# Optimization experiments

Hardware: AMD Instinct MI355X
Metric: run time of the kernel (lower is better)

The kernel has to match this reference:

```python
import jax, jax.numpy as jnp
import numpy as np

B, C, H, W = 4, 32, 64, 64
K = 3
HEADS = 8
SF = 4
D = C * K * K          # 288, unfold token dim
E = D // 2             # 144, reduced dim
DH = E // HEADS        # 18, head dim
SCALE = DH ** -0.5
N = H * W              # 4096 tokens


def unfold(x):
    # x: (B,C,H,W) -> (B, C*K*K, H*W), torch.nn.Unfold ordering (c, kh, kw)
    xp = jnp.pad(x, ((0, 0), (0, 0), (1, 1), (1, 1)))
    patches = jnp.stack([xp[:, :, i:i + H, j:j + W] for i in range(K) for j in range(K)], axis=2)
    return patches.reshape(x.shape[0], C * K * K, H * W)


def fold(cols):
    # inverse of unfold: scatter-add overlapping patches back, crop padding
    b = cols.shape[0]
    y = cols.reshape(b, C, K, K, H, W)
    out = jnp.zeros((b, C, H + 2, W + 2), cols.dtype)
    for i in range(K):
        for j in range(K):
            out = out.at[:, :, i:i + H, j:j + W].add(y[:, :, i, j])
    return out[:, :, 1:-1, 1:-1]


def layernorm_cols(cols, g, b):
    # LayerNorm over D applied on (B,N,D) view, returned as (B,D,N)
    xt = cols.transpose(0, 2, 1)
    mu = xt.mean(-1, keepdims=True)
    var = xt.var(-1, keepdims=True)
    y = (xt - mu) / jnp.sqrt(var + 1e-5) * g + b
    return y.transpose(0, 2, 1)


def emha(x, wr, br, wqkv, we, be):
    # x: (B, D, N)
    b, _, n_tok = x.shape
    xr = jnp.einsum('bdn,ed->ben', x, wr) + br[None, :, None]   # Conv1d k=1 reduction
    t = xr.transpose(0, 2, 1)                                   # (B,N,E)
    qkv = t @ wqkv.T                                            # Linear, no bias
    q, k, v = jnp.split(qkv, 3, axis=-1)
    n = n_tok // SF

    def rs(a):
        return a.reshape(b, n_tok, HEADS, DH).transpose(0, 2, 1, 3).reshape(b, HEADS, SF, n, DH)

    q, k, v = rs(q), rs(k), rs(v)
    attn = jax.nn.softmax(jnp.einsum('bhsnd,bhsmd->bhsnm', q, k) * SCALE, axis=-1)
    o = jnp.einsum('bhsnm,bhsmd->bhsnd', attn, v)
    o = o.reshape(b, HEADS, n_tok, DH).transpose(0, 2, 1, 3).reshape(b, n_tok, E).transpose(0, 2, 1)
    return jnp.einsum('ben,fe->bfn', o, we) + be[None, :, None]  # Conv1d k=1 expansion


def conv3x3(x, w, b):
    y = jax.lax.conv_general_dilated(x, w, (1, 1), ((1, 1), (1, 1)),
                                     dimension_numbers=('NCHW', 'OIHW', 'NCHW'))
    return y + b[None, :, None, None]


def setup_inputs() -> dict:
    key = jax.random.key(0)
    ks = jax.random.split(key, 20)
    s = 0.02
    inp = {
        'x': jax.random.normal(ks[0], (B, C, H, W), jnp.float32),
        'ln_g': jnp.ones((D,), jnp.float32),
        'ln_b': jnp.zeros((D,), jnp.float32),
        'conv_w': jax.random.normal(ks[1], (C, C, 3, 3), jnp.float32) * s,
        'conv_b': jnp.zeros((C,), jnp.float32),
    }
    for i in range(3):
        k0, k1, k2 = jax.random.split(ks[2 + i], 3)
        inp[f'wr{i+1}'] = jax.random.normal(k0, (E, D), jnp.float32) * s
        inp[f'br{i+1}'] = jnp.zeros((E,), jnp.float32)
        inp[f'wqkv{i+1}'] = jax.random.normal(k1, (3 * E, E), jnp.float32) * s
        inp[f'we{i+1}'] = jax.random.normal(k2, (D, E), jnp.float32) * s
        inp[f'be{i+1}'] = jnp.zeros((D,), jnp.float32)
    return inp


def reference(x, ln_g, ln_b, conv_w, conv_b,
              wr1, br1, wqkv1, we1, be1,
              wr2, br2, wqkv2, we2, be2,
              wr3, br3, wqkv3, we3, be3):
    t = x
    for (wr, br, wqkv, we, be) in ((wr1, br1, wqkv1, we1, be1),
                                   (wr2, br2, wqkv2, we2, be2),
                                   (wr3, br3, wqkv3, we3, be3)):
        cols = unfold(t)
        cols_n = layernorm_cols(cols, ln_g, ln_b)
        cols = emha(cols_n, wr, br, wqkv, we, be) + cols
        t = fold(cols)
    return x + jax.nn.elu(conv3x3(t, conv_w, conv_b))
```

## Files before the change

kernel.cpp:

```cpp
#include <hip/hip_runtime.h>
#include <math.h>

#define BN 4
#define CC 32
#define HH 64
#define WW 64
#define DD 288
#define EE 144
#define NTOK 4096
#define SCALE_F 0.2357022603955158f
#define QSCALE  0.3401074286f
#define QKST 384
#define MQKV 528

typedef __bf16 bf16x8 __attribute__((ext_vector_type(8)));
typedef float floatx4 __attribute__((ext_vector_type(4)));
typedef unsigned short u16x8 __attribute__((ext_vector_type(8)));

__device__ __forceinline__ unsigned short f2bf(float x) {
    unsigned int u = __float_as_uint(x);
    u += 0x7fffu + ((u >> 16) & 1u);
    return (unsigned short)(u >> 16);
}
__device__ __forceinline__ float bf2f(unsigned short s) {
    return __uint_as_float(((unsigned int)s) << 16);
}
__device__ __forceinline__ unsigned int pack_bf_trunc(float a, float b) {
    return __builtin_amdgcn_perm(__float_as_uint(b), __float_as_uint(a), 0x07060302u);
}
__device__ __forceinline__ void plswap32(unsigned int& a, unsigned int& b) {
    asm("v_permlane32_swap_b32 %0, %1" : "+v"(a), "+v"(b));
}
__device__ __forceinline__ void plswap16(unsigned int& a, unsigned int& b) {
    asm("v_permlane16_swap_b32 %0, %1" : "+v"(a), "+v"(b));
}

__global__ __launch_bounds__(256) void setup_k(
    const float* __restrict__ wr0, const float* __restrict__ br0,
    const float* __restrict__ wr1, const float* __restrict__ br1,
    const float* __restrict__ wr2, const float* __restrict__ br2,
    const float* __restrict__ g,  const float* __restrict__ lb,
    const float* __restrict__ wqkv0, const float* __restrict__ wqkv1, const float* __restrict__ wqkv2,
    const float* __restrict__ we0,   const float* __restrict__ we1,   const float* __restrict__ we2,
    unsigned short* __restrict__ wg_bf, float* __restrict__ wgsum, float* __restrict__ wbeta,
    unsigned short* __restrict__ wqkv_bf, unsigned short* __restrict__ we_bf)
{
    int blk = blockIdx.x;
    int tid = threadIdx.x;
    if (blk < 3) {
        if (tid < 144) {
            int l = blk, e = tid;
            const float* wr = (l == 0) ? wr0 : ((l == 1) ? wr1 : wr2);
            const float* br = (l == 0) ? br0 : ((l == 1) ? br1 : br2);
            float sg = 0.f, sb = 0.f;
            for (int d = 0; d < DD; ++d) {
                float w = wr[e * DD + d];
                float wgv = w * g[d];
                wg_bf[((size_t)l * EE + e) * DD + d] = f2bf(wgv);
                sg += wgv;
                sb += w * lb[d];
            }
            wgsum[l * EE + e] = sg;
            wbeta[l * EE + e] = sb + br[e];
        }
        return;
    }
    int idx = (blk - 3) * 256 + tid;
    const int T1 = 3 * MQKV * 160;
    const int T2 = 3 * 288 * 160;
    if (idx < T1) {
        int l = idx / (MQKV * 160), r = idx % (MQKV * 160);
        int m = r / 160, k = r % 160;
        const float* w = (l == 0) ? wqkv0 : ((l == 1) ? wqkv1 : wqkv2);
        float v = 0.f;
        if (k < 144) {
            if (m < 192) {
                int h = m / 24, j = m % 24;
                if (j < 18) v = w[(h * 18 + j) * 144 + k] * QSCALE;
            } else if (m < 384) {
                int mm = m - 192, h = mm / 24, j = mm % 24;
                if (j < 18) v = w[(144 + h * 18 + j) * 144 + k];
            } else {
                v = w[(288 + (m - 384)) * 144 + k];
            }
        }
        wqkv_bf[idx] = f2bf(v);
    } else if (idx < T1 + T2) {
        int j = idx - T1;
        int l = j / (288 * 160), r = j % (288 * 160);
        int m = r / 160, k = r % 160;
        const float* w = (l == 0) ? we0 : ((l == 1) ? we1 : we2);
        we_bf[j] = (k < 144) ? f2bf(w[m * 144 + k]) : 0;
    }
}

__global__ __launch_bounds__(256) void unfold_k(const float* __restrict__ t,
    unsigned short* __restrict__ colsT,
    float* __restrict__ mu, float* __restrict__ rstd)
{
    __shared__ float red1[4][64], red2[4][64];
    int tid = threadIdx.x;
    int lane = tid & 63, cpart = tid >> 6;
    int b = blockIdx.x >> 6, nc = blockIdx.x & 63;
    int n = nc * 64 + lane;
    int h = n >> 6, w = n & 63;
    const float* tb = t + (size_t)b * CC * HH * WW;
    unsigned short loc[72];
    float s1 = 0.f, s2 = 0.f;
    #pragma unroll
    for (int c8 = 0; c8 < 8; ++c8) {
        int c = cpart * 8 + c8;
        const float* tc = tb + (size_t)c * 4096;
        #pragma unroll
        for (int i = 0; i < 3; ++i) {
            int hr = h + i - 1;
            bool rok = ((unsigned)hr < 64u);
            #pragma unroll
            for (int j = 0; j < 3; ++j) {
                int wc = w + j - 1;
                bool ok = rok && ((unsigned)wc < 64u);
                float v = ok ? tc[hr * 64 + wc] : 0.f;
                loc[c8 * 9 + i * 3 + j] = f2bf(v);
                s1 += v;
                s2 = fmaf(v, v, s2);
            }
        }
    }
    unsigned short* ct = colsT + ((size_t)b * NTOK + n) * 288 + cpart * 72;
    #pragma unroll
    for (int u = 0; u < 9; ++u)
        *(u16x8*)&ct[u * 8] = *(const u16x8*)&loc[u * 8];
    red1[cpart][lane] = s1;
    red2[cpart][lane] = s2;
    __syncthreads();
    if (tid < 64) {
        float a = red1[0][tid] + red1[1][tid] + red1[2][tid] + red1[3][tid];
        float q = red2[0][tid] + red2[1][tid] + red2[2][tid] + red2[3][tid];
        float m = a * (1.f / 288.f);
        float var = q * (1.f / 288.f) - m * m;
        int nn = nc * 64 + tid;
        mu[b * NTOK + nn] = m;
        rstd[b * NTOK + nn] = rsqrtf(var + 1e-5f);
    }
}

template<int K, int MODE, int NYB>
__global__ __launch_bounds__(256) void mgemm_k(
    const unsigned short* __restrict__ A, const unsigned short* __restrict__ Bt, int BST,
    unsigned short* __restrict__ Ct, unsigned short* __restrict__ Cv,
    const float* __restrict__ mu, const float* __restrict__ rstd,
    const float* __restrict__ wgsum, const float* __restrict__ wbeta,
    const float* __restrict__ bias)
{
    constexpr int NT = 64;
    __shared__ unsigned short Ts[64 * 56];
    int flat = blockIdx.x;
    int g  = (flat / (8 * NYB)) * 8 + (flat & 7);
    int jm = (flat % (8 * NYB)) >> 3;
    int n0 = (g & 63) * NT;
    int bI = g >> 6;
    int m0 = jm * 48;
    int tid = threadIdx.x;
    int wv = tid >> 6, lane = tid & 63;
    int l15 = lane & 15, l4 = lane >> 4;

    const unsigned short* Arow = A + (size_t)(m0 + l15) * K + l4 * 8;
    const unsigned short* Brow = Bt + ((size_t)bI * NTOK + n0 + wv * 16 + l15) * BST + l4 * 8;

    floatx4 acc[3];
    acc[0] = acc[1] = acc[2] = (floatx4){0.f, 0.f, 0.f, 0.f};

    #pragma unroll
    for (int ks = 0; ks < K / 32; ++ks) {
        bf16x8 bfr = *(const bf16x8*)(Brow + ks * 32);
        #pragma unroll
        for (int mi = 0; mi < 3; ++mi) {
            bf16x8 af = *(const bf16x8*)(Arow + (size_t)mi * 16 * K + ks * 32);
            acc[mi] = __builtin_amdgcn_mfma_f32_16x16x32_bf16(af, bfr, acc[mi], 0, 0, 0);
        }
    }

    int n_l = wv * 16 + l15;

    if (MODE == 2) {
        #pragma unroll
        for (int mi = 0; mi < 3; ++mi)
            #pragma unroll
            for (int r = 0; r < 4; ++r) {
                int m_l = mi * 16 + l4 * 4 + r;
                Ts[m_l * 72 + n_l] = f2bf(acc[mi][r] + bias[m0 + m_l]);
            }
        __syncthreads();
        for (int u = tid; u < 48 * 8; u += 256) {
            int row = u >> 3, seg = u & 7;
            unsigned short* dst = Ct + ((size_t)bI * DD + m0 + row) * NTOK + n0 + seg * 8;
            *(u16x8*)dst = *(const u16x8*)&Ts[row * 72 + seg * 8];
        }
    } else {
        bool vpath = (MODE == 0) && (m0 >= 384);
        float muv = 0.f, rsv = 0.f;
        if (MODE == 1) {
            int n_g = n0 + n_l;
            muv = mu[bI * NTOK + n_g];
            rsv = rstd[bI * NTOK + n_g];
        }
        #pragma unroll
        for (int mi = 0; mi < 3; ++mi)
            #pragma unroll
            for (int r = 0; r < 4; ++r) {
                int m_l = mi * 16 + l4 * 4 + r;
                float v = acc[mi][r];
                if (MODE == 1) v = rsv * (v - muv * wgsum[m0 + m_l]) + wbeta[m0 + m_l];
                if (!vpath) Ts[n_l * 56 + m_l] = f2bf(v);
                else        Ts[m_l * 72 + n_l] = f2bf(v);
            }
        __syncthreads();
        if (!vpath) {
            const int CTS = (MODE == 1) ? 160 : QKST;
            if (tid < 128) {
                int row = tid >> 1, half = tid & 1;
                unsigned short* dst = Ct + ((size_t)bI * NTOK + n0 + row) * CTS + m0 + half * 24;
                const unsigned short* src = &Ts[row * 56 + half * 24];
                #pragma unroll
                for (int u = 0; u < 3; ++u)
                    *(u16x8*)&dst[u * 8] = *(const u16x8*)&src[u * 8];
                if (MODE == 1 && m0 == 96) {
                    u16x8 z = (u16x8)0;
                    *(u16x8*)(Ct + ((size_t)bI * NTOK + n0 + row) * 160 + 144 + half * 8) = z;
                }
            }
        } else {
            for (int u = tid; u < 48 * 8; u += 256) {
                int row = u >> 3, seg = u & 7;
                unsigned short* dst = Cv + ((size_t)bI * EE + (m0 - 384) + row) * NTOK + n0 + seg * 8;
                *(u16x8*)dst = *(const u16x8*)&Ts[row * 72 + seg * 8];
            }
        }
    }
}

__global__ __launch_bounds__(256, 6) void attn_k2(const unsigned short* __restrict__ qkT,
                                                  const unsigned short* __restrict__ vF,
                                                  unsigned short* __restrict__ oT)
{
    __shared__ unsigned short Ks[128 * 40];
    __shared__ unsigned short Vs[32 * 136];

    int blk = blockIdx.x;
    int bhs = blk & 127;
    int qc  = blk >> 7;
    int b = bhs >> 5, h = (bhs >> 2) & 7, s = bhs & 3;
    int tid  = threadIdx.x;
    int wv   = tid >> 6;
    int lane = tid & 63;
    int l15 = lane & 15, l4 = lane >> 4;
    int q0 = qc * 64;
    int tokbase = s * 1024;

    const unsigned short* qkb = qkT + (size_t)b * NTOK * QKST;

    if (tid < 128) {
        u16x8 z = (u16x8)0;
        *(u16x8*)&Ks[tid * 40 + 24] = z;
    } else {
        for (int v = tid - 128; v < 14 * 16; v += 128) {
            int d = 18 + (v >> 4), seg = v & 15;
            unsigned short val = (d == 31) ? (unsigned short)0x3F80 : (unsigned short)0;
            u16x8 vv = (u16x8)val;
            *(u16x8*)&Vs[d * 136 + seg * 8] = vv;
        }
    }

    bf16x8 qf;
    {
        u16x8 raw = *(const u16x8*)(qkb + (size_t)(tokbase + q0 + wv * 16 + l15) * QKST
                                    + 24 * h + l4 * 8);
        if (l4 == 3) raw = (u16x8)0;
        qf = *(bf16x8*)&raw;
    }

    floatx4 oacc[2];
    oacc[0] = (floatx4){0.f, 0.f, 0.f, 0.f};
    oacc[1] = (floatx4){0.f, 0.f, 0.f, 0.f};

    u16x8 preg[3];
    int vb = tid - 128;
    bool v3 = (vb < 32);
    if (tid < 128) {
        const unsigned short* src = qkb + (size_t)(tokbase + tid) * QKST + 192 + 24 * h;
        preg[0] = *(const u16x8*)&src[0];
        preg[1] = *(const u16x8*)&src[8];
        preg[2] = *(const u16x8*)&src[16];
    } else {
        const unsigned short* vbb = vF + (size_t)b * EE * NTOK + tokbase;
        #pragma unroll
        for (int u = 0; u < 3; ++u) {
            int idx = vb + u * 128;
            if (u < 2 || v3) {
                int d = idx >> 4, seg = idx & 15;
                preg[u] = *(const u16x8*)(vbb + (size_t)(h * 18 + d) * NTOK + seg * 8);
            }
        }
    }

    for (int c0 = 0; c0 < 1024; c0 += 128) {
        __syncthreads();
        if (tid < 128) {
            unsigned short* dk = &Ks[tid * 40];
            *(u16x8*)&dk[0]  = preg[0];
            *(u16x8*)&dk[8]  = preg[1];
            *(u16x8*)&dk[16] = preg[2];
        } else {
            #pragma unroll
            for (int u = 0; u < 3; ++u) {
                int idx = vb + u * 128;
                if (u < 2 || v3) {
                    int d = idx >> 4, seg = idx & 15;
                    *(u16x8*)&Vs[d * 136 + seg * 8] = preg[u];
                }
            }
        }
        int cn = c0 + 128;
        if (cn < 1024) {
            if (tid < 128) {
                const unsigned short* src = qkb + (size_t)(tokbase + cn + tid) * QKST + 192 + 24 * h;
                preg[0] = *(const u16x8*)&src[0];
                preg[1] = *(const u16x8*)&src[8];
                preg[2] = *(const u16x8*)&src[16];
            } else {
                const unsigned short* vbb = vF + (size_t)b * EE * NTOK + tokbase + cn;
                #pragma unroll
                for (int u = 0; u < 3; ++u) {
                    int idx = vb + u * 128;
                    if (u < 2 || v3) {
                        int d = idx >> 4, seg = idx & 15;
                        preg[u] = *(const u16x8*)(vbb + (size_t)(h * 18 + d) * NTOK + seg * 8);
                    }
                }
            }
        }
        __syncthreads();

        #pragma unroll
        for (int sub = 0; sub < 2; ++sub) {
            bf16x8 kf[4];
            #pragma unroll
            for (int mi = 0; mi < 4; ++mi)
                kf[mi] = *(const bf16x8*)&Ks[(sub * 64 + mi * 16 + l15) * 40 + l4 * 8];

            floatx4 sacc[4];
            #pragma unroll
            for (int mi = 0; mi < 4; ++mi) {
                floatx4 z = (floatx4){0.f, 0.f, 0.f, 0.f};
                sacc[mi] = __builtin_amdgcn_mfma_f32_16x16x32_bf16(kf[mi], qf, z, 0, 0, 0);
            }

            unsigned int pk0[4], pk1[4];
            #pragma unroll
            for (int mi = 0; mi < 4; ++mi) {
                pk0[mi] = pack_bf_trunc(exp2f(sacc[mi][0]), exp2f(sacc[mi][1]));
                pk1[mi] = pack_bf_trunc(exp2f(sacc[mi][2]), exp2f(sacc[mi][3]));
            }

            #pragma unroll
            for (int c = 0; c < 2; ++c) {
                unsigned int B0 = pk0[2 * c], B2 = pk0[2 * c + 1];
                unsigned int B1 = pk1[2 * c], B3 = pk1[2 * c + 1];
                plswap32(B0, B2); plswap16(B0, B2);
                plswap32(B1, B3); plswap16(B1, B3);
                union { unsigned int u[4]; bf16x8 v; } bfr;
                bfr.u[0] = B0; bfr.u[1] = B1; bfr.u[2] = B2; bfr.u[3] = B3;
                #pragma unroll
                for (int nd = 0; nd < 2; ++nd) {
                    bf16x8 af = *(const bf16x8*)&Vs[(nd * 16 + l15) * 136 + sub * 64 + c * 32 + l4 * 8];
                    oacc[nd] = __builtin_amdgcn_mfma_f32_16x16x32_bf16(af, bfr.v, oacc[nd], 0, 0, 0);
                }
            }
        }
    }

    float lsum = __shfl(oacc[1][3], 48 + l15, 64);
    float inv  = 1.f / lsum;
    size_t rowi = (size_t)b * NTOK + tokbase + q0 + wv * 16 + l15;
    unsigned short* orow = oT + rowi * 160 + h * 18;
    unsigned int w0 = (unsigned)f2bf(oacc[0][0] * inv) | ((unsigned)f2bf(oacc[0][1] * inv) << 16);
    unsigned int w1 = (unsigned)f2bf(oacc[0][2] * inv) | ((unsigned)f2bf(oacc[0][3] * inv) << 16);
    *(unsigned int*)&orow[l4 * 4]     = w0;
    *(unsigned int*)&orow[l4 * 4 + 2] = w1;
    if (l4 == 0) {
        unsigned int w2 = (unsigned)f2bf(oacc[1][0] * inv) | ((unsigned)f2bf(oacc[1][1] * inv) << 16);
        *(unsigned int*)&orow[16] = w2;
    }
    if (h == 7 && l4 < 2) {
        u16x8 z = (u16x8)0;
        *(u16x8*)(oT + rowi * 160 + 144 + l4 * 8) = z;
    }
}

__global__ __launch_bounds__(256) void fold_k(const unsigned short* __restrict__ cols,
                                              const float* __restrict__ tprev,
                                              float* __restrict__ t)
{
    int idx = blockIdx.x * 256 + threadIdx.x;
    int w = idx & 63;
    int h = (idx >> 6) & 63;
    int c = (idx >> 12) & 31;
    int b = idx >> 17;
    const unsigned short* cb = cols + (size_t)b * DD * NTOK + (size_t)c * 9 * NTOK;
    float sum = 0.f;
    #pragma unroll
    for (int i = 0; i < 3; ++i) {
        int hs = h + 1 - i;
        if ((unsigned)hs < 64u) {
            #pragma unroll
            for (int j = 0; j < 3; ++j) {
                int ws_ = w + 1 - j;
                if ((unsigned)ws_ < 64u)
                    sum += bf2f(cb[(size_t)(i * 3 + j) * NTOK + hs * 64 + ws_]);
            }
        }
    }
    int ch = (h == 0 || h == 63) ? 2 : 3;
    int cw_ = (w == 0 || w == 63) ? 2 : 3;
    t[idx] = sum + (float)(ch * cw_) * tprev[idx];
}

__global__ __launch_bounds__(256) void conv_k(const float* __restrict__ t,
    const float* __restrict__ cw, const float* __restrict__ cbias,
    const float* __restrict__ x, float* __restrict__ out)
{
    __shared__ float wsh[CC * 9];
    int blk = blockIdx.x;
    int band = blk & 3, co = (blk >> 2) & 31, b = blk >> 7;
    int tid = threadIdx.x;
    for (int u = tid; u < CC * 9; u += 256) wsh[u] = cw[co * CC * 9 + u];
    __syncthreads();
    int h = band * 16 + (tid >> 4);
    int w0 = (tid & 15) << 2;
    const float* tb = t + (size_t)b * CC * 4096;
    float bias = cbias[co];
    float a0 = bias, a1 = bias, a2 = bias, a3 = bias;
    for (int ci = 0; ci < CC; ++ci) {
        const float* tc = tb + (size_t)ci * 4096;
        const float* wr = &wsh[ci * 9];
        #pragma unroll
        for (int i = 0; i < 3; ++i) {
            int hr = h + i - 1;
            if ((unsigned)hr < 64u) {
                const float* row = tc + hr * 64;
                float vl = (w0 > 0)  ? row[w0 - 1] : 0.f;
                float4 c4 = *(const float4*)&row[w0];
                float vr = (w0 < 60) ? row[w0 + 4] : 0.f;
                float wj0 = wr[i * 3], wj1 = wr[i * 3 + 1], wj2 = wr[i * 3 + 2];
                a0 = fmaf(wj0, vl,   a0); a0 = fmaf(wj1, c4.x, a0); a0 = fmaf(wj2, c4.y, a0);
                a1 = fmaf(wj0, c4.x, a1); a1 = fmaf(wj1, c4.y, a1); a1 = fmaf(wj2, c4.z, a1);
                a2 = fmaf(wj0, c4.y, a2); a2 = fmaf(wj1, c4.z, a2); a2 = fmaf(wj2, c4.w, a2);
                a3 = fmaf(wj0, c4.z, a3); a3 = fmaf(wj1, c4.w, a3); a3 = fmaf(wj2, vr,   a3);
            }
        }
    }
    size_t oidx = ((size_t)(b * CC + co) * 4096) + h * 64 + w0;
    float4 xin = *(const float4*)&x[oidx];
    float4 o;
    o.x = xin.x + ((a0 > 0.f) ? a0 : (__expf(a0) - 1.f));
    o.y = xin.y + ((a1 > 0.f) ? a1 : (__expf(a1) - 1.f));
    o.z = xin.z + ((a2 > 0.f) ? a2 : (__expf(a2) - 1.f));
    o.w = xin.w + ((a3 > 0.f) ? a3 : (__expf(a3) - 1.f));
    *(float4*)&out[oidx] = o;
}

extern "C" void kernel_launch(void* const* d_in, const int* in_sizes, int n_in,
                              void* d_out, int out_size, void* d_ws, size_t ws_size,
                              hipStream_t stream)
{
    const float* x    = (const float*)d_in[0];
    const float* ln_g = (const float*)d_in[1];
    const float* ln_b = (const float*)d_in[2];
    const float* cw   = (const float*)d_in[3];
    const float* cb   = (const float*)d_in[4];
    const float* wr[3]   = {(const float*)d_in[5],  (const float*)d_in[10], (const float*)d_in[15]};
    const float* br[3]   = {(const float*)d_in[6],  (const float*)d_in[11], (const float*)d_in[16]};
    const float* wqkv[3] = {(const float*)d_in[7],  (const float*)d_in[12], (const float*)d_in[17]};
    const float* we[3]   = {(const float*)d_in[8],  (const float*)d_in[13], (const float*)d_in[18]};
    const float* be[3]   = {(const float*)d_in[9],  (const float*)d_in[14], (const float*)d_in[19]};
    float* out = (float*)d_out;

    char* p = (char*)d_ws;
    unsigned short* cols_bf = (unsigned short*)p; p += (size_t)BN * DD * NTOK * 2;
    unsigned short* colsT = (unsigned short*)p; p += (size_t)BN * NTOK * 288 * 2;
    unsigned short* oT = colsT;
    unsigned short* xrT   = (unsigned short*)p; p += (size_t)BN * NTOK * 160 * 2;
    unsigned short* qkT   = (unsigned short*)p; p += (size_t)BN * NTOK * QKST * 2;
    unsigned short* vF    = (unsigned short*)p; p += (size_t)BN * EE * NTOK * 2;
    float* mu   = (float*)p;              p += (size_t)BN * NTOK * 4;
    float* rstd = (float*)p;              p += (size_t)BN * NTOK * 4;
    float* tA   = (float*)p;              p += (size_t)BN * CC * HH * WW * 4;
    float* tB   = (float*)p;              p += (size_t)BN * CC * HH * WW * 4;
    unsigned short* wg_bf   = (unsigned short*)p; p += (size_t)3 * EE * DD * 2;
    unsigned short* wqkv_bf = (unsigned short*)p; p += (size_t)3 * MQKV * 160 * 2;
    unsigned short* we_bf   = (unsigned short*)p; p += (size_t)3 * DD * 160 * 2;
    float* wgsum = (float*)p;             p += 3 * EE * 4;
    float* wbeta = (float*)p;             p += 3 * EE * 4;
    (void)in_sizes; (void)n_in; (void)out_size; (void)ws_size;

    setup_k<<<1533, 256, 0, stream>>>(wr[0], br[0], wr[1], br[1], wr[2], br[2], ln_g, ln_b,
                                      wqkv[0], wqkv[1], wqkv[2], we[0], we[1], we[2],
                                      wg_bf, wgsum, wbeta, wqkv_bf, we_bf);

    const float* tin = x;
    float* touts[3] = {tA, tB, tA};
    for (int l = 0; l < 3; ++l) {
        unfold_k<<<256, 256, 0, stream>>>(tin, colsT, mu, rstd);
        mgemm_k<288, 1, 3><<<768, 256, 0, stream>>>(
            wg_bf + (size_t)l * EE * DD, colsT, 288, xrT, nullptr,
            mu, rstd, wgsum + l * EE, wbeta + l * EE, nullptr);
        mgemm_k<160, 0, 11><<<2816, 256, 0, stream>>>(
            wqkv_bf + (size_t)l * MQKV * 160, xrT, 160, qkT, vF,
            nullptr, nullptr, nullptr, nullptr, nullptr);
        attn_k2<<<2048, 256, 0, stream>>>(qkT, vF, oT);
        mgemm_k<160, 2, 6><<<1536, 256, 0, stream>>>(
            we_bf + (size_t)l * DD * 160, oT, 160, cols_bf, nullptr,
            nullptr, nullptr, nullptr, nullptr, be[l]);
        fold_k<<<2048, 256, 0, stream>>>(cols_bf, tin, touts[l]);
        tin = touts[l];
    }
    conv_k<<<512, 256, 0, stream>>>(tA, cw, cb, x, out);
}
```

Before: 432.1 us.

## Store K in per-head padded layout and load K fragments directly from global

The QKV GEMM now writes K into a separate per-(batch,head) buffer with a 32-element padded row, and Q into its own narrower buffer. The attention kernel reads K MFMA fragments straight from global memory into registers instead of staging them through shared memory, so only V goes through LDS and the K LDS buffer disappears. It also swaps exp2f for the hardware exp2 intrinsic and lowers the launch-bounds occupancy hint from 6 to 4 to make room for the extra registers. The cost is more global-load traffic per wave, since each of the four waves in a block re-reads the same K, and possibly lower occupancy.

```diff
diff --git a/kernel.cpp b/kernel.cpp
--- a/kernel.cpp
+++ b/kernel.cpp
@@ -10,7 +10,8 @@
 #define NTOK 4096
 #define SCALE_F 0.2357022603955158f
 #define QSCALE  0.3401074286f
-#define QKST 384
+#define QST 192
+#define KST 32
 #define MQKV 528
 
 typedef __bf16 bf16x8 __attribute__((ext_vector_type(8)));
@@ -147,7 +148,7 @@
 template<int K, int MODE, int NYB>
 __global__ __launch_bounds__(256) void mgemm_k(
     const unsigned short* __restrict__ A, const unsigned short* __restrict__ Bt, int BST,
-    unsigned short* __restrict__ Ct, unsigned short* __restrict__ Cv,
+    unsigned short* __restrict__ Ct, unsigned short* __restrict__ Cv, unsigned short* __restrict__ Ck,
     const float* __restrict__ mu, const float* __restrict__ rstd,
     const float* __restrict__ wgsum, const float* __restrict__ wbeta,
     const float* __restrict__ bias)
@@ -216,17 +217,26 @@
             }
         __syncthreads();
         if (!vpath) {
-            const int CTS = (MODE == 1) ? 160 : QKST;
             if (tid < 128) {
                 int row = tid >> 1, half = tid & 1;
-                unsigned short* dst = Ct + ((size_t)bI * NTOK + n0 + row) * CTS + m0 + half * 24;
                 const unsigned short* src = &Ts[row * 56 + half * 24];
-                #pragma unroll
-                for (int u = 0; u < 3; ++u)
-                    *(u16x8*)&dst[u * 8] = *(const u16x8*)&src[u * 8];
-                if (MODE == 1 && m0 == 96) {
-                    u16x8 z = (u16x8)0;
-                    *(u16x8*)(Ct + ((size_t)bI * NTOK + n0 + row) * 160 + 144 + half * 8) = z;
+                if (MODE == 0 && m0 >= 192) {
+                    int head = (m0 - 192) / 24 + half;
+                    unsigned short* dst = Ck + ((size_t)(bI * 8 + head) * NTOK + n0 + row) * KST;
+                    #pragma unroll
+                    for (int u = 0; u < 3; ++u)
+                        *(u16x8*)&dst[u * 8] = *(const u16x8*)&src[u * 8];
+                    *(u16x8*)&dst[24] = (u16x8)0;
+                } else {
+                    const int CTS = (MODE == 1) ? 160 : QST;
+                    unsigned short* dst = Ct + ((size_t)bI * NTOK + n0 + row) * CTS + m0 + half * 24;
+                    #pragma unroll
+                    for (int u = 0; u < 3; ++u)
+                        *(u16x8*)&dst[u * 8] = *(const u16x8*)&src[u * 8];
+                    if (MODE == 1 && m0 == 96) {
+                        u16x8 z = (u16x8)0;
+                        *(u16x8*)(Ct + ((size_t)bI * NTOK + n0 + row) * 160 + 144 + half * 8) = z;
+                    }
                 }
             }
         } else {
@@ -239,11 +249,11 @@
     }
 }
 
-__global__ __launch_bounds__(256, 6) void attn_k2(const unsigned short* __restrict__ qkT,
+__global__ __launch_bounds__(256, 4) void attn_k2(const unsigned short* __restrict__ qT,
+                                                  const unsigned short* __restrict__ kP,
                                                   const unsigned short* __restrict__ vF,
                                                   unsigned short* __restrict__ oT)
 {
-    __shared__ unsigned short Ks[128 * 40];
     __shared__ unsigned short Vs[32 * 136];
 
     int blk = blockIdx.x;
@@ -257,23 +267,16 @@
     int q0 = qc * 64;
     int tokbase = s * 1024;
 
-    const unsigned short* qkb = qkT + (size_t)b * NTOK * QKST;
-
-    if (tid < 128) {
-        u16x8 z = (u16x8)0;
-        *(u16x8*)&Ks[tid * 40 + 24] = z;
-    } else {
-        for (int v = tid - 128; v < 14 * 16; v += 128) {
-            int d = 18 + (v >> 4), seg = v & 15;
-            unsigned short val = (d == 31) ? (unsigned short)0x3F80 : (unsigned short)0;
-            u16x8 vv = (u16x8)val;
-            *(u16x8*)&Vs[d * 136 + seg * 8] = vv;
-        }
+    for (int v = tid; v < 14 * 16; v += 256) {
+        int d = 18 + (v >> 4), seg = v & 15;
+        unsigned short val = (d == 31) ? (unsigned short)0x3F80 : (unsigned short)0;
+        u16x8 vv = (u16x8)val;
+        *(u16x8*)&Vs[d * 136 + seg * 8] = vv;
     }
 
     bf16x8 qf;
     {
-        u16x8 raw = *(const u16x8*)(qkb + (size_t)(tokbase + q0 + wv * 16 + l15) * QKST
+        u16x8 raw = *(const u16x8*)(qT + ((size_t)b * NTOK + tokbase + q0 + wv * 16 + l15) * QST
                                     + 24 * h + l4 * 8);
         if (l4 == 3) raw = (u16x8)0;
         qf = *(bf16x8*)&raw;
@@ -283,83 +286,52 @@
     oacc[0] = (floatx4){0.f, 0.f, 0.f, 0.f};
     oacc[1] = (floatx4){0.f, 0.f, 0.f, 0.f};
 
-    u16x8 preg[3];
-    int vb = tid - 128;
-    bool v3 = (vb < 32);
-    if (tid < 128) {
-        const unsigned short* src = qkb + (size_t)(tokbase + tid) * QKST + 192 + 24 * h;
-        preg[0] = *(const u16x8*)&src[0];
-        preg[1] = *(const u16x8*)&src[8];
-        preg[2] = *(const u16x8*)&src[16];
-    } else {
-        const unsigned short* vbb = vF + (size_t)b * EE * NTOK + tokbase;
-        #pragma unroll
-        for (int u = 0; u < 3; ++u) {
-            int idx = vb + u * 128;
-            if (u < 2 || v3) {
-                int d = idx >> 4, seg = idx & 15;
-                preg[u] = *(const u16x8*)(vbb + (size_t)(h * 18 + d) * NTOK + seg * 8);
-            }
-        }
-    }
+    const unsigned short* vbb = vF + (size_t)b * EE * NTOK + tokbase;
+    int d0 = tid >> 4, seg0 = tid & 15;
+    bool x2 = (tid < 32);
+    int d1 = 16 + (tid >> 4), seg1 = tid & 15;
+    u16x8 pv0, pv1;
+    pv0 = *(const u16x8*)(vbb + (size_t)(h * 18 + d0) * NTOK + seg0 * 8);
+    if (x2) pv1 = *(const u16x8*)(vbb + (size_t)(h * 18 + d1) * NTOK + seg1 * 8);
+
+    const unsigned short* kRow = kP + ((size_t)(b * 8 + h) * NTOK + tokbase + l15) * KST + l4 * 8;
 
     for (int c0 = 0; c0 < 1024; c0 += 128) {
+        bf16x8 kreg[8];
+        #pragma unroll
+        for (int sub = 0; sub < 2; ++sub)
+            #pragma unroll
+            for (int mi = 0; mi < 4; ++mi) {
+                u16x8 raw = *(const u16x8*)(kRow + (unsigned)(c0 + sub * 64 + mi * 16) * KST);
+                kreg[sub * 4 + mi] = *(bf16x8*)&raw;
+            }
+
         __syncthreads();
-        if (tid < 128) {
-            unsigned short* dk = &Ks[tid * 40];
-            *(u16x8*)&dk[0]  = preg[0];
-            *(u16x8*)&dk[8]  = preg[1];
-            *(u16x8*)&dk[16] = preg[2];
-        } else {
-            #pragma unroll
-            for (int u = 0; u < 3; ++u) {
-                int idx = vb + u * 128;
-                if (u < 2 || v3) {
-                    int d = idx >> 4, seg = idx & 15;
-                    *(u16x8*)&Vs[d * 136 + seg * 8] = preg[u];
-                }
-            }
-        }
+        *(u16x8*)&Vs[d0 * 136 + seg0 * 8] = pv0;
+        if (x2) *(u16x8*)&Vs[d1 * 136 + seg1 * 8] = pv1;
         int cn = c0 + 128;
         if (cn < 1024) {
-            if (tid < 128) {
-                const unsigned short* src = qkb + (size_t)(tokbase + cn + tid) * QKST + 192 + 24 * h;
-                preg[0] = *(const u16x8*)&src[0];
-                preg[1] = *(const u16x8*)&src[8];
-                preg[2] = *(const u16x8*)&src[16];
-            } else {
-                const unsigned short* vbb = vF + (size_t)b * EE * NTOK + tokbase + cn;
-                #pragma unroll
-                for (int u = 0; u < 3; ++u) {
-                    int idx = vb + u * 128;
-                    if (u < 2 || v3) {
-                        int d = idx >> 4, seg = idx & 15;
-                        preg[u] = *(const u16x8*)(vbb + (size_t)(h * 18 + d) * NTOK + seg * 8);
-                    }
-                }
-            }
+            pv0 = *(const u16x8*)(vbb + (size_t)(h * 18 + d0) * NTOK + cn + seg0 * 8);
+            if (x2) pv1 = *(const u16x8*)(vbb + (size_t)(h * 18 + d1) * NTOK + cn + seg1 * 8);
         }
         __syncthreads();
 
         #pragma unroll
         for (int sub = 0; sub < 2; ++sub) {
-            bf16x8 kf[4];
-            #pragma unroll
-            for (int mi = 0; mi < 4; ++mi)
-                kf[mi] = *(const bf16x8*)&Ks[(sub * 64 + mi * 16 + l15) * 40 + l4 * 8];
-
             floatx4 sacc[4];
             #pragma unroll
             for (int mi = 0; mi < 4; ++mi) {
                 floatx4 z = (floatx4){0.f, 0.f, 0.f, 0.f};
-                sacc[mi] = __builtin_amdgcn_mfma_f32_16x16x32_bf16(kf[mi], qf, z, 0, 0, 0);
+                sacc[mi] = __builtin_amdgcn_mfma_f32_16x16x32_bf16(kreg[sub * 4 + mi], qf, z, 0, 0, 0);
             }
 
             unsigned int pk0[4], pk1[4];
             #pragma unroll
             for (int mi = 0; mi < 4; ++mi) {
-                pk0[mi] = pack_bf_trunc(exp2f(sacc[mi][0]), exp2f(sacc[mi][1]));
-                pk1[mi] = pack_bf_trunc(exp2f(sacc[mi][2]), exp2f(sacc[mi][3]));
+                pk0[mi] = pack_bf_trunc(__builtin_amdgcn_exp2f(sacc[mi][0]),
+                                        __builtin_amdgcn_exp2f(sacc[mi][1]));
+                pk1[mi] = pack_bf_trunc(__builtin_amdgcn_exp2f(sacc[mi][2]),
+                                        __builtin_amdgcn_exp2f(sacc[mi][3]));
             }
 
             #pragma unroll
@@ -490,7 +462,8 @@
     unsigned short* colsT = (unsigned short*)p; p += (size_t)BN * NTOK * 288 * 2;
     unsigned short* oT = colsT;
     unsigned short* xrT   = (unsigned short*)p; p += (size_t)BN * NTOK * 160 * 2;
-    unsigned short* qkT   = (unsigned short*)p; p += (size_t)BN * NTOK * QKST * 2;
+    unsigned short* qT    = (unsigned short*)p; p += (size_t)BN * NTOK * QST * 2;
+    unsigned short* kP    = (unsigned short*)p; p += (size_t)BN * 8 * NTOK * KST * 2;
     unsigned short* vF    = (unsigned short*)p; p += (size_t)BN * EE * NTOK * 2;
     float* mu   = (float*)p;              p += (size_t)BN * NTOK * 4;
     float* rstd = (float*)p;              p += (size_t)BN * NTOK * 4;
@@ -512,14 +485,14 @@
     for (int l = 0; l < 3; ++l) {
         unfold_k<<<256, 256, 0, stream>>>(tin, colsT, mu, rstd);
         mgemm_k<288, 1, 3><<<768, 256, 0, stream>>>(
-            wg_bf + (size_t)l * EE * DD, colsT, 288, xrT, nullptr,
+            wg_bf + (size_t)l * EE * DD, colsT, 288, xrT, nullptr, nullptr,
             mu, rstd, wgsum + l * EE, wbeta + l * EE, nullptr);
         mgemm_k<160, 0, 11><<<2816, 256, 0, stream>>>(
-            wqkv_bf + (size_t)l * MQKV * 160, xrT, 160, qkT, vF,
+            wqkv_bf + (size_t)l * MQKV * 160, xrT, 160, qT, vF, kP,
             nullptr, nullptr, nullptr, nullptr, nullptr);
-        attn_k2<<<2048, 256, 0, stream>>>(qkT, vF, oT);
+        attn_k2<<<2048, 256, 0, stream>>>(qT, kP, vF, oT);
         mgemm_k<160, 2, 6><<<1536, 256, 0, stream>>>(
-            we_bf + (size_t)l * DD * 160, oT, 160, cols_bf, nullptr,
+            we_bf + (size_t)l * DD * 160, oT, 160, cols_bf, nullptr, nullptr,
             nullptr, nullptr, nullptr, nullptr, be[l]);
         fold_k<<<2048, 256, 0, stream>>>(cols_bf, tin, touts[l]);
         tin = touts[l];
```

After: 420.7 us. 1.03x faster.
